# Optimization experiments

Hardware: AMD Instinct MI355X
Metric: run time of the kernel (lower is better)

Reference implementation:

```python
import jax, jax.numpy as jnp
import numpy as np

K = 3          # kernel_size
OUT = 128      # out_channels
PAD = K // 2   # padding


def setup_inputs() -> dict:
    key = jax.random.key(0)
    k1, k2 = jax.random.split(key)
    x = jax.random.normal(k1, (32, 128, 56, 56), dtype=jnp.float32)
    # FilterStripe weight: [K*K*out_channels, in_channels] (1x1 trailing dims dropped)
    weight = jax.random.normal(k2, (K * K * OUT, 128), dtype=jnp.float32) * 0.05
    return {"x": x, "weight": weight}


def reference(x, weight):
    # The torch forward does: unfold(K, pad=K//2) -> view(b,c,K*K,h,w) -> permute to
    # (b, K*K, c, h, w) -> grouped 1x1 conv with groups=K*K -> sum over the K*K axis.
    # Group g corresponds to kernel tap (kh, kw) with g = kh*K + kw, using filters
    # weight[g*out:(g+1)*out]. Summing over g is exactly a standard KxK convolution
    # with OIHW kernel w[o, c, kh, kw] = weight[(kh*K + kw)*out + o, c].
    in_ch = x.shape[1]
    w = weight.reshape(K, K, OUT, in_ch).transpose(2, 3, 0, 1)  # [out, in, K, K]
    return jax.lax.conv_general_dilated(
        x, w,
        window_strides=(1, 1),
        padding=((PAD, PAD), (PAD, PAD)),
        dimension_numbers=("NCHW", "OIHW", "NCHW"),
    )
```

## Files before the change

kernel.cpp:

```cpp
#include <hip/hip_runtime.h>
#include <hip/hip_bf16.h>

typedef __bf16 bf16x8 __attribute__((ext_vector_type(8)));
typedef float  f32x4  __attribute__((ext_vector_type(4)));

#define HW       3136
#define IMG_W    56
#define IMG_H    56
#define WGRAN    (9*128*16)
#define WB_BYTES ((size_t)WGRAN*16)
#define CBLK     224

#define AS1 __attribute__((address_space(1)))
#define AS3 __attribute__((address_space(3)))

__global__ __launch_bounds__(256) void wcvt_kernel(const float* __restrict__ w,
                                                   unsigned char* __restrict__ wb) {
    int i = blockIdx.x * 256 + threadIdx.x;
    if (i >= WGRAN) return;
    const int l15 = i & 15, lq = (i >> 4) & 3, f = (i >> 6) & 1;
    const int c   = (i >> 7) & 3, q32 = (i >> 9) & 3, tap = i >> 11;
    const int oc = q32 * 32 + f * 16 + l15;
    const int ch = c * 32 + lq * 8;
    const float* src = w + (size_t)(tap * 128 + oc) * 128 + ch;
    bf16x8 v;
    #pragma unroll
    for (int j = 0; j < 8; ++j) v[j] = (__bf16)src[j];
    *(bf16x8*)(wb + (size_t)i * 16) = v;
}

__device__ __forceinline__ void stage_task(unsigned char* xs, const float* __restrict__ xn,
                                           int obase, int s, int cg, int lane) {
    const int ar  = obase - 1 + s;
    const int arc = min(max(ar, 0), IMG_H - 1);
    const int wcc = min(max(lane - 1, 0), IMG_W - 1);
    const bool v  = (ar >= 0) & (ar < IMG_H) & (lane >= 1) & (lane <= IMG_W);
    const float* bp = xn + (size_t)(cg * 8) * HW + arc * IMG_W + wcc;
    bf16x8 pk;
    #pragma unroll
    for (int j = 0; j < 8; ++j) {
        float f = bp[(size_t)j * HW];
        pk[j] = (__bf16)(v ? f : 0.f);
    }
    *(bf16x8*)(xs + s * 16384 + lane * 256 + ((cg ^ (lane & 7)) * 16)) = pk;
}

template<bool STG>
__device__ __forceinline__ void compute_tile(unsigned char* xs, const __bf16* wt,
                                             float* on, int oc0, int g7, int tloc,
                                             int obase, int lane,
                                             const float* __restrict__ xn, int wv) {
    const int l15 = lane & 15, lq = lane >> 4;
    int vb[7], pr_[7], pc_[7];
    #pragma unroll
    for (int k = 0; k < 7; ++k) {
        int p = (g7 * 7 + k) * 16 + l15;
        int pr = p / 56, pc = p - pr * 56;
        pr_[k] = pr; pc_[k] = pc;
        vb[k] = (4 * tloc + pr + 1) * 16384 + (pc + 1) * 256;
    }
    f32x4 acc[2][7];
    #pragma unroll
    for (int f = 0; f < 2; ++f)
        #pragma unroll
        for (int k = 0; k < 7; ++k) acc[f][k] = (f32x4){0.f, 0.f, 0.f, 0.f};

    #pragma unroll
    for (int tap = 0; tap < 9; ++tap) {
        bf16x8 a[8];
        const __bf16* wn = wt + tap * 16384;
        #pragma unroll
        for (int i = 0; i < 8; ++i)
            a[i] = *(const bf16x8*)(wn + ((i & 3) * 2 + (i >> 2)) * 512);
        if (STG && tap == 2) {
            #pragma unroll
            for (int i = 0; i < 4; ++i) {
                int tid = 96 + wv + 8 * i;
                stage_task(xs, xn, obase, 6 + ((tid - 96) >> 4), (tid - 96) & 15, lane);
            }
        }
        if (STG && tap == 4) {
            #pragma unroll
            for (int i = 4; i < 8; ++i) {
                int tid = 96 + wv + 8 * i;
                stage_task(xs, xn, obase, 6 + ((tid - 96) >> 4), (tid - 96) & 15, lane);
            }
        }
        __builtin_amdgcn_sched_barrier(0);

        const int dh = tap / 3 - 1, dw = tap - (tap / 3) * 3 - 1;
        const int offb = dh * 16384 + dw * 256;
        int sw[7];
        #pragma unroll
        for (int k = 0; k < 7; ++k) sw[k] = (pc_[k] + 1 + dw) & 7;

        __builtin_amdgcn_s_setprio(1);
        #pragma unroll
        for (int c = 0; c < 4; ++c) {
            #pragma unroll
            for (int k = 0; k < 7; ++k) {
                int gi = ((c * 4 + lq) ^ sw[k]) * 16;
                bf16x8 b = *(const bf16x8*)(xs + vb[k] + offb + gi);
                acc[0][k] = __builtin_amdgcn_mfma_f32_16x16x32_bf16(a[c],     b, acc[0][k], 0, 0, 0);
                acc[1][k] = __builtin_amdgcn_mfma_f32_16x16x32_bf16(a[4 + c], b, acc[1][k], 0, 0, 0);
            }
        }
        __builtin_amdgcn_s_setprio(0);
        __builtin_amdgcn_sched_barrier(0);
    }

    #pragma unroll
    for (int f = 0; f < 2; ++f)
        #pragma unroll
        for (int k = 0; k < 7; ++k) {
            int pos = (obase + 4 * tloc + pr_[k]) * 56 + pc_[k];
            int oc  = oc0 + f * 16 + lq * 4;
            #pragma unroll
            for (int rr = 0; rr < 4; ++rr)
                on[(size_t)(oc + rr) * HW + pos] = acc[f][k][rr];
        }
}

__global__ __launch_bounds__(512, 2) void conv_kernel(const float* __restrict__ x,
                                                      const unsigned char* __restrict__ wb,
                                                      float* __restrict__ out) {
    __shared__ __align__(16) unsigned char xs[163840];
    const int t = threadIdx.x, lane = t & 63, wv = t >> 6;
    const int b = blockIdx.x;
    const int swz = (b & 7) * 28 + (b >> 3);
    const int img = swz / 7, loc = swz - img * 7;
    const int obase = loc * 8;

    const float* xn = x + (size_t)img * 128 * HW;

    #pragma unroll 3
    for (int i = 0; i < 12; ++i) {
        int tid = wv + 8 * i;
        stage_task(xs, xn, obase, tid >> 4, tid & 15, lane);
    }
    __syncthreads();

    const int oc0 = (wv & 3) * 32;
    const int g7  = wv >> 2;
    const __bf16* wt = (const __bf16*)(wb + (size_t)(wv & 3) * 8192 + lane * 16);
    float* on = out + (size_t)img * 128 * HW;

    compute_tile<true>(xs, wt, on, oc0, g7, 0, obase, lane, xn, wv);

    __syncthreads();

    compute_tile<false>(xs, wt, on, oc0, g7, 1, obase, lane, xn, wv);
}

#define PITCH  272
#define LDSB   (4*64*PITCH)
#define NBLK   896

template<int NPF>
__device__ __forceinline__ void fb_compute(const unsigned char* xs, const float* wf,
                                           float* on, int oc0, int pf0, int r0, int lane) {
    const int l15 = lane & 15, lq = lane >> 4;
    int spb[NPF];
    #pragma unroll
    for (int k = 0; k < NPF; ++k) {
        int p = (pf0 + k) * 16 + l15;
        int r = p / 56, w = p - r * 56;
        spb[k] = ((r + 1) * 64 + (w + 1)) * PITCH + lq * 16;
    }
    f32x4 acc[2][NPF];
    #pragma unroll
    for (int f = 0; f < 2; ++f)
        #pragma unroll
        for (int k = 0; k < NPF; ++k) acc[f][k] = (f32x4){0.f, 0.f, 0.f, 0.f};
    #pragma unroll 3
    for (int tap = 0; tap < 9; ++tap) {
        const int offb  = ((tap / 3) * 64 + (tap % 3) - 65) * PITCH;
        const int wbase = tap * 16384 + oc0 * 128 + l15 * 128 + lq * 8;
        #pragma unroll
        for (int c = 0; c < 4; ++c) {
            bf16x8 a[2];
            #pragma unroll
            for (int f = 0; f < 2; ++f) {
                const float* p = wf + wbase + f * 2048 + c * 32;
                #pragma unroll
                for (int j = 0; j < 8; ++j) a[f][j] = (__bf16)p[j];
            }
            #pragma unroll
            for (int k = 0; k < NPF; ++k) {
                bf16x8 b = *(const bf16x8*)(xs + spb[k] + offb + c * 64);
                #pragma unroll
                for (int f = 0; f < 2; ++f)
                    acc[f][k] = __builtin_amdgcn_mfma_f32_16x16x32_bf16(a[f], b, acc[f][k], 0, 0, 0);
            }
        }
    }
    #pragma unroll
    for (int f = 0; f < 2; ++f)
        #pragma unroll
        for (int k = 0; k < NPF; ++k) {
            int pos = r0 * 56 + (pf0 + k) * 16 + l15;
            int oc  = oc0 + f * 16 + lq * 4;
            #pragma unroll
            for (int rr = 0; rr < 4; ++rr)
                on[(size_t)(oc + rr) * HW + pos] = acc[f][k][rr];
        }
}

__global__ __launch_bounds__(512, 4) void fb_conv_kernel(const float* __restrict__ x,
                                                         const float* __restrict__ wf,
                                                         float* __restrict__ out) {
    __shared__ __align__(16) unsigned char xs[LDSB];
    const int tid = threadIdx.x, lane = tid & 63, wv = tid >> 6;
    const int bid = blockIdx.x;
    const int swz = (bid & 7) * (NBLK / 8) + (bid >> 3);
    const int n = swz / 28, rp = swz - n * 28, r0 = rp * 2;
    if (wv < 4) {
        const float* xn = x + (size_t)n * 128 * HW;
        const int ar = r0 - 1 + wv, wi = lane - 1;
        const bool v = (ar >= 0) & (ar < IMG_H) & (wi >= 0) & (wi < IMG_W);
        const int gc = min(max(ar, 0), IMG_H - 1) * IMG_W + min(max(wi, 0), IMG_W - 1);
        unsigned char* dst = xs + (wv * 64 + lane) * PITCH;
        #pragma unroll
        for (int cg = 0; cg < 16; ++cg) {
            bf16x8 pk;
            #pragma unroll
            for (int j = 0; j < 8; ++j) {
                float f = xn[(size_t)(cg * 8 + j) * HW + gc];
                pk[j] = (__bf16)(v ? f : 0.f);
            }
            *(bf16x8*)(dst + cg * 16) = pk;
        }
    }
    __syncthreads();
    const int oc0 = (wv & 3) * 32;
    float* on = out + (size_t)n * 128 * HW;
    if (wv < 4) fb_compute<4>(xs, wf, on, oc0, 0, r0, lane);
    else        fb_compute<3>(xs, wf, on, oc0, 4, r0, lane);
}

extern "C" void kernel_launch(void* const* d_in, const int* in_sizes, int n_in,
                              void* d_out, int out_size, void* d_ws, size_t ws_size,
                              hipStream_t stream) {
    const float* x = (const float*)d_in[0];
    const float* w = (const float*)d_in[1];
    float* out = (float*)d_out;

    if (ws_size >= WB_BYTES) {
        unsigned char* wb = (unsigned char*)d_ws;
        wcvt_kernel<<<(WGRAN + 255) / 256, 256, 0, stream>>>(w, wb);
        conv_kernel<<<CBLK, 512, 0, stream>>>(x, wb, out);
    } else {
        fb_conv_kernel<<<NBLK, 512, 0, stream>>>(x, w, out);
    }
}
```

Baseline: 50.33 us.

## Shrink conv tiles to 4 rows with channel-halved LDS staging for higher occupancy

```diff
diff --git a/kernel.cpp b/kernel.cpp
--- a/kernel.cpp
+++ b/kernel.cpp
@@ -9,7 +9,9 @@
 #define IMG_H    56
 #define WGRAN    (9*128*16)
 #define WB_BYTES ((size_t)WGRAN*16)
-#define CBLK     224
+#define CBLK     448
+#define SLOT_B   9216
+#define LDS_B    (6*SLOT_B)
 
 #define AS1 __attribute__((address_space(1)))
 #define AS3 __attribute__((address_space(3)))
@@ -29,36 +31,81 @@
     *(bf16x8*)(wb + (size_t)i * 16) = v;
 }
 
+template<int H>
 __device__ __forceinline__ void stage_task(unsigned char* xs, const float* __restrict__ xn,
-                                           int obase, int s, int cg, int lane) {
+                                           int obase, int s, int g, int lane) {
     const int ar  = obase - 1 + s;
     const int arc = min(max(ar, 0), IMG_H - 1);
     const int wcc = min(max(lane - 1, 0), IMG_W - 1);
     const bool v  = (ar >= 0) & (ar < IMG_H) & (lane >= 1) & (lane <= IMG_W);
-    const float* bp = xn + (size_t)(cg * 8) * HW + arc * IMG_W + wcc;
+    const float* bp = xn + (size_t)(H * 64 + g * 8) * HW + arc * IMG_W + wcc;
     bf16x8 pk;
     #pragma unroll
     for (int j = 0; j < 8; ++j) {
         float f = bp[(size_t)j * HW];
         pk[j] = (__bf16)(v ? f : 0.f);
     }
-    *(bf16x8*)(xs + s * 16384 + lane * 256 + ((cg ^ (lane & 7)) * 16)) = pk;
-}
-
-template<bool STG>
-__device__ __forceinline__ void compute_tile(unsigned char* xs, const __bf16* wt,
-                                             float* on, int oc0, int g7, int tloc,
-                                             int obase, int lane,
-                                             const float* __restrict__ xn, int wv) {
+    *(bf16x8*)(xs + s * SLOT_B + lane * 144 + g * 16) = pk;
+}
+
+template<int H>
+__device__ __forceinline__ void compute_half(const unsigned char* xs, const unsigned char* wt,
+                                             f32x4 acc[2][7], const int vb[7], int lq) {
+    bf16x8 aB[2][2];
+    #pragma unroll
+    for (int f = 0; f < 2; ++f)
+        aB[0][f] = *(const bf16x8*)(wt + ((H * 2) * 2 + f) * 1024);
+
+    #pragma unroll
+    for (int s = 0; s < 18; ++s) {
+        const int tap = s >> 1, cl = s & 1;
+        if (s < 17) {
+            const int t2 = (s + 1) >> 1, c2 = (s + 1) & 1;
+            #pragma unroll
+            for (int f = 0; f < 2; ++f)
+                aB[(s + 1) & 1][f] = *(const bf16x8*)(wt + t2 * 32768
+                                                      + ((H * 2 + c2) * 2 + f) * 1024);
+        }
+        __builtin_amdgcn_sched_barrier(0);
+
+        const int dh = tap / 3 - 1, dw = tap - (tap / 3) * 3 - 1;
+        const int offb = dh * SLOT_B + dw * 144 + (cl * 4 + lq) * 16;
+        __builtin_amdgcn_s_setprio(1);
+        #pragma unroll
+        for (int k = 0; k < 7; ++k) {
+            bf16x8 b = *(const bf16x8*)(xs + vb[k] + offb);
+            acc[0][k] = __builtin_amdgcn_mfma_f32_16x16x32_bf16(aB[s & 1][0], b, acc[0][k], 0, 0, 0);
+            acc[1][k] = __builtin_amdgcn_mfma_f32_16x16x32_bf16(aB[s & 1][1], b, acc[1][k], 0, 0, 0);
+        }
+        __builtin_amdgcn_s_setprio(0);
+        __builtin_amdgcn_sched_barrier(0);
+    }
+}
+
+__global__ __launch_bounds__(512, 4) void conv_kernel(const float* __restrict__ x,
+                                                      const unsigned char* __restrict__ wb,
+                                                      float* __restrict__ out) {
+    __shared__ __align__(16) unsigned char xs[LDS_B];
+    const int t = threadIdx.x, lane = t & 63, wv = t >> 6;
     const int l15 = lane & 15, lq = lane >> 4;
-    int vb[7], pr_[7], pc_[7];
+    const int b = blockIdx.x;
+    const int swz = (b & 7) * 56 + (b >> 3);
+    const int img = swz / 14, loc = swz - img * 14;
+    const int obase = loc * 4;
+
+    const float* xn = x + (size_t)img * 128 * HW;
+    const int q32 = wv & 3;
+    const int g7  = wv >> 2;
+    const unsigned char* wt = wb + (size_t)q32 * 8192 + lane * 16;
+
+    int vb[7];
     #pragma unroll
     for (int k = 0; k < 7; ++k) {
         int p = (g7 * 7 + k) * 16 + l15;
         int pr = p / 56, pc = p - pr * 56;
-        pr_[k] = pr; pc_[k] = pc;
-        vb[k] = (4 * tloc + pr + 1) * 16384 + (pc + 1) * 256;
-    }
+        vb[k] = (pr + 1) * SLOT_B + (pc + 1) * 144;
+    }
+
     f32x4 acc[2][7];
     #pragma unroll
     for (int f = 0; f < 2; ++f)
@@ -66,90 +113,35 @@
         for (int k = 0; k < 7; ++k) acc[f][k] = (f32x4){0.f, 0.f, 0.f, 0.f};
 
     #pragma unroll
-    for (int tap = 0; tap < 9; ++tap) {
-        bf16x8 a[8];
-        const __bf16* wn = wt + tap * 16384;
-        #pragma unroll
-        for (int i = 0; i < 8; ++i)
-            a[i] = *(const bf16x8*)(wn + ((i & 3) * 2 + (i >> 2)) * 512);
-        if (STG && tap == 2) {
-            #pragma unroll
-            for (int i = 0; i < 4; ++i) {
-                int tid = 96 + wv + 8 * i;
-                stage_task(xs, xn, obase, 6 + ((tid - 96) >> 4), (tid - 96) & 15, lane);
-            }
-        }
-        if (STG && tap == 4) {
-            #pragma unroll
-            for (int i = 4; i < 8; ++i) {
-                int tid = 96 + wv + 8 * i;
-                stage_task(xs, xn, obase, 6 + ((tid - 96) >> 4), (tid - 96) & 15, lane);
-            }
-        }
-        __builtin_amdgcn_sched_barrier(0);
-
-        const int dh = tap / 3 - 1, dw = tap - (tap / 3) * 3 - 1;
-        const int offb = dh * 16384 + dw * 256;
-        int sw[7];
-        #pragma unroll
-        for (int k = 0; k < 7; ++k) sw[k] = (pc_[k] + 1 + dw) & 7;
-
-        __builtin_amdgcn_s_setprio(1);
-        #pragma unroll
-        for (int c = 0; c < 4; ++c) {
-            #pragma unroll
-            for (int k = 0; k < 7; ++k) {
-                int gi = ((c * 4 + lq) ^ sw[k]) * 16;
-                bf16x8 b = *(const bf16x8*)(xs + vb[k] + offb + gi);
-                acc[0][k] = __builtin_amdgcn_mfma_f32_16x16x32_bf16(a[c],     b, acc[0][k], 0, 0, 0);
-                acc[1][k] = __builtin_amdgcn_mfma_f32_16x16x32_bf16(a[4 + c], b, acc[1][k], 0, 0, 0);
-            }
-        }
-        __builtin_amdgcn_s_setprio(0);
-        __builtin_amdgcn_sched_barrier(0);
-    }
-
+    for (int i = 0; i < 6; ++i) {
+        int task = wv + 8 * i;
+        stage_task<0>(xs, xn, obase, task >> 3, task & 7, lane);
+    }
+    __syncthreads();
+    compute_half<0>(xs, wt, acc, vb, lq);
+    __syncthreads();
+
+    #pragma unroll
+    for (int i = 0; i < 6; ++i) {
+        int task = wv + 8 * i;
+        stage_task<1>(xs, xn, obase, task >> 3, task & 7, lane);
+    }
+    __syncthreads();
+    compute_half<1>(xs, wt, acc, vb, lq);
+
+    float* on = out + (size_t)img * 128 * HW;
     #pragma unroll
     for (int f = 0; f < 2; ++f)
         #pragma unroll
         for (int k = 0; k < 7; ++k) {
-            int pos = (obase + 4 * tloc + pr_[k]) * 56 + pc_[k];
-            int oc  = oc0 + f * 16 + lq * 4;
+            int p = (g7 * 7 + k) * 16 + l15;
+            int pr = p / 56, pc = p - pr * 56;
+            int pos = (obase + pr) * 56 + pc;
+            int oc  = q32 * 32 + f * 16 + lq * 4;
             #pragma unroll
             for (int rr = 0; rr < 4; ++rr)
                 on[(size_t)(oc + rr) * HW + pos] = acc[f][k][rr];
         }
-}
-
-__global__ __launch_bounds__(512, 2) void conv_kernel(const float* __restrict__ x,
-                                                      const unsigned char* __restrict__ wb,
-                                                      float* __restrict__ out) {
-    __shared__ __align__(16) unsigned char xs[163840];
-    const int t = threadIdx.x, lane = t & 63, wv = t >> 6;
-    const int b = blockIdx.x;
-    const int swz = (b & 7) * 28 + (b >> 3);
-    const int img = swz / 7, loc = swz - img * 7;
-    const int obase = loc * 8;
-
-    const float* xn = x + (size_t)img * 128 * HW;
-
-    #pragma unroll 3
-    for (int i = 0; i < 12; ++i) {
-        int tid = wv + 8 * i;
-        stage_task(xs, xn, obase, tid >> 4, tid & 15, lane);
-    }
-    __syncthreads();
-
-    const int oc0 = (wv & 3) * 32;
-    const int g7  = wv >> 2;
-    const __bf16* wt = (const __bf16*)(wb + (size_t)(wv & 3) * 8192 + lane * 16);
-    float* on = out + (size_t)img * 128 * HW;
-
-    compute_tile<true>(xs, wt, on, oc0, g7, 0, obase, lane, xn, wv);
-
-    __syncthreads();
-
-    compute_tile<false>(xs, wt, on, oc0, g7, 1, obase, lane, xn, wv);
 }
 
 #define PITCH  272
```

Measured after the change: 49.07 us (median of 2 runs). -2.5%, faster.
